# Kernel optimization log

Measured on AMD Instinct MI355X. Metric: run time of the kernel, lower is better.

## Reference

```python
import jax, jax.numpy as jnp
import numpy as np

N = 131072
K = 1024
D = 64

def setup_inputs() -> dict:
    key = jax.random.key(0)
    k1, k2 = jax.random.split(key)
    x = jax.random.normal(k1, (N, D), dtype=jnp.float32)
    emb_weight = jax.random.normal(k2, (K, D), dtype=jnp.float32)
    return {"x": x, "emb_weight": emb_weight}

def reference(x, emb_weight):
    distances = (
        jnp.sum(x * x, axis=1, keepdims=True)
        + jnp.sum(emb_weight * emb_weight, axis=1)
        - 2.0 * jnp.matmul(x, emb_weight.T)
    )
    codebook_indices = jnp.argmin(distances, axis=1)  # [N]
    probs = jax.nn.one_hot(codebook_indices, K, dtype=x.dtype)  # [N, K]
    z_q = emb_weight[codebook_indices]  # [N, D]
    return (z_q, probs)
```

## Files before the change

### kernel.cpp

```cpp
#include <hip/hip_runtime.h>
#include <math.h>

#define N_TOK 131072
#define K_CB  1024
#define D_DIM 64
#define MARGIN 0.03f

#define WS_EN     0
#define WS_ES     4096
#define WS_CNT    266240
#define WS_LIST   266256

typedef short bf16x8 __attribute__((ext_vector_type(8)));
typedef float f32x4  __attribute__((ext_vector_type(4)));

__device__ __forceinline__ ushort f2bf(float f) {
    uint u = __float_as_uint(f);
    u += 0x7FFFu + ((u >> 16) & 1u);
    return (ushort)(u >> 16);
}
__device__ __forceinline__ float bf2f(ushort h) {
    return __uint_as_float(((uint)h) << 16);
}

__global__ __launch_bounds__(256) void prep_fill(
    const float* __restrict__ emb, float* __restrict__ en,
    ushort* __restrict__ es, uint* __restrict__ fixcnt,
    float* __restrict__ probs)
{
    const int tid = threadIdx.x;
    const int b   = blockIdx.x;

    {
        const f32x4 z = {0.f, 0.f, 0.f, 0.f};
        f32x4* p = (f32x4*)probs + (size_t)b * 16384 + tid;
        #pragma unroll
        for (int i = 0; i < 64; ++i) p[(size_t)i * 256] = z;
    }

    if (b >= 16) return;

    const int c6   = tid & 63;
    const int q    = tid >> 6;
    const int code = b * 64 + c6;
    if (b == 0 && tid == 0) *fixcnt = 0;

    const int cb = code >> 4, jj = code & 15;
    const float* er = emb + (size_t)code * D_DIM;
    #pragma unroll
    for (int j = 0; j < 16; ++j) {
        int d = q * 16 + j;
        float f = er[d];
        ushort h = f2bf(f);
        ushort l = f2bf(f - bf2f(h));
        int ks = d >> 5, quad = (d >> 3) & 3, e = d & 7;
        es[(size_t)(((cb * 4 + ks)     * 4 + quad) * 16 + jj) * 8 + e] = h;
        es[(size_t)(((cb * 4 + ks + 2) * 4 + quad) * 16 + jj) * 8 + e] = l;
    }
    if (q == 0) {
        float s = 0.f;
        #pragma unroll
        for (int d = 0; d < D_DIM; ++d) s = fmaf(er[d], er[d], s);
        en[code] = s;
    }
}

__global__ __launch_bounds__(256) void vq_onehot(
    const float* __restrict__ x, const float* __restrict__ emb,
    const float* __restrict__ en, const ushort* __restrict__ es,
    float* __restrict__ zq, float* __restrict__ probs,
    uint* __restrict__ fixcnt, uint* __restrict__ fixlist, uint fixcap)
{
    const int tid  = threadIdx.x;
    const int wave = tid >> 6, lane = tid & 63;
    const int quad = lane >> 4, l15 = lane & 15;
    const int rg = wave >> 1;
    const int h  = wave & 1;
    const int blockRow = blockIdx.x * 64;
    const int waveRowBase = blockRow + rg * 32;

    __shared__ float lds_b1[2][64];
    __shared__ float lds_b2[2][64];
    __shared__ int   lds_k1[2][64];
    __shared__ int   lds_bk[64];

    bf16x8 af[2][4];
    #pragma unroll
    for (int g = 0; g < 2; ++g) {
        const float* xr = x + (size_t)(waveRowBase + g * 16 + l15) * D_DIM + quad * 8;
        f32x4 p0 = *(const f32x4*)(xr);
        f32x4 p1 = *(const f32x4*)(xr + 4);
        f32x4 p2 = *(const f32x4*)(xr + 32);
        f32x4 p3 = *(const f32x4*)(xr + 36);
        float v0[8], v1[8];
        #pragma unroll
        for (int j = 0; j < 4; ++j) { v0[j] = p0[j]; v0[4 + j] = p1[j]; v1[j] = p2[j]; v1[4 + j] = p3[j]; }
        #pragma unroll
        for (int j = 0; j < 8; ++j) {
            ushort h0 = f2bf(v0[j]);
            af[g][0][j] = (short)h0;
            af[g][2][j] = (short)f2bf(v0[j] - bf2f(h0));
            ushort h1 = f2bf(v1[j]);
            af[g][1][j] = (short)h1;
            af[g][3][j] = (short)f2bf(v1[j] - bf2f(h1));
        }
    }

    float b1[8], b2[8]; int k1[8];
    #pragma unroll
    for (int s = 0; s < 8; ++s) { b1[s] = INFINITY; b2[s] = INFINITY; k1[s] = 0; }

    const bf16x8* __restrict__ esv = (const bf16x8*)es;
    const int fidx = quad * 16 + l15;
    const int cb0  = h * 32;

    bf16x8 bc[4]; float enc;
    #pragma unroll
    for (int ks = 0; ks < 4; ++ks) bc[ks] = esv[(size_t)cb0 * 256 + ks * 64 + fidx];
    enc = en[cb0 * 16 + l15];

    #pragma unroll 2
    for (int i = 0; i < 32; ++i) {
        const int cb  = cb0 + i;
        const int nbi = cb0 + ((i + 1) & 31);
        bf16x8 bn[4]; float enn;
        #pragma unroll
        for (int ks = 0; ks < 4; ++ks) bn[ks] = esv[(size_t)nbi * 256 + ks * 64 + fidx];
        enn = en[nbi * 16 + l15];

        f32x4 acc0 = {0.f, 0.f, 0.f, 0.f};
        f32x4 acc1 = {0.f, 0.f, 0.f, 0.f};
        acc0 = __builtin_amdgcn_mfma_f32_16x16x32_bf16(af[0][0], bc[0], acc0, 0, 0, 0);
        acc0 = __builtin_amdgcn_mfma_f32_16x16x32_bf16(af[0][1], bc[1], acc0, 0, 0, 0);
        acc0 = __builtin_amdgcn_mfma_f32_16x16x32_bf16(af[0][0], bc[2], acc0, 0, 0, 0);
        acc0 = __builtin_amdgcn_mfma_f32_16x16x32_bf16(af[0][1], bc[3], acc0, 0, 0, 0);
        acc0 = __builtin_amdgcn_mfma_f32_16x16x32_bf16(af[0][2], bc[0], acc0, 0, 0, 0);
        acc0 = __builtin_amdgcn_mfma_f32_16x16x32_bf16(af[0][3], bc[1], acc0, 0, 0, 0);
        acc1 = __builtin_amdgcn_mfma_f32_16x16x32_bf16(af[1][0], bc[0], acc1, 0, 0, 0);
        acc1 = __builtin_amdgcn_mfma_f32_16x16x32_bf16(af[1][1], bc[1], acc1, 0, 0, 0);
        acc1 = __builtin_amdgcn_mfma_f32_16x16x32_bf16(af[1][0], bc[2], acc1, 0, 0, 0);
        acc1 = __builtin_amdgcn_mfma_f32_16x16x32_bf16(af[1][1], bc[3], acc1, 0, 0, 0);
        acc1 = __builtin_amdgcn_mfma_f32_16x16x32_bf16(af[1][2], bc[0], acc1, 0, 0, 0);
        acc1 = __builtin_amdgcn_mfma_f32_16x16x32_bf16(af[1][3], bc[1], acc1, 0, 0, 0);

        const int code = cb * 16 + l15;
        #pragma unroll
        for (int r = 0; r < 4; ++r) {
            {
                float d = fmaf(-2.f, acc0[r], enc);
                bool lt = d < b1[r];
                b2[r] = lt ? b1[r] : fminf(b2[r], d);
                k1[r] = lt ? code : k1[r];
                b1[r] = lt ? d : b1[r];
            }
            {
                int s = 4 + r;
                float d = fmaf(-2.f, acc1[r], enc);
                bool lt = d < b1[s];
                b2[s] = lt ? b1[s] : fminf(b2[s], d);
                k1[s] = lt ? code : k1[s];
                b1[s] = lt ? d : b1[s];
            }
        }

        #pragma unroll
        for (int ks = 0; ks < 4; ++ks) bc[ks] = bn[ks];
        enc = enn;
    }

    #pragma unroll
    for (int s = 0; s < 8; ++s) {
        #pragma unroll
        for (int off = 1; off < 16; off <<= 1) {
            float ob1 = __shfl_xor(b1[s], off);
            int   ok1 = __shfl_xor(k1[s], off);
            float ob2 = __shfl_xor(b2[s], off);
            bool better = (ob1 < b1[s]) || (ob1 == b1[s] && ok1 < k1[s]);
            float loser = better ? b1[s] : ob1;
            b1[s] = better ? ob1 : b1[s];
            k1[s] = better ? ok1 : k1[s];
            b2[s] = fminf(fminf(b2[s], ob2), loser);
        }
    }

    if (l15 == 0) {
        #pragma unroll
        for (int s = 0; s < 8; ++s) {
            int idx = rg * 32 + (s >> 2) * 16 + quad * 4 + (s & 3);
            lds_b1[h][idx] = b1[s];
            lds_b2[h][idx] = b2[s];
            lds_k1[h][idx] = k1[s];
        }
    }
    __syncthreads();

    if (tid < 64) {
        float a1 = lds_b1[0][tid], a2 = lds_b2[0][tid]; int ak = lds_k1[0][tid];
        float c1 = lds_b1[1][tid], c2 = lds_b2[1][tid]; int ck = lds_k1[1][tid];
        bool bwin = c1 < a1;
        float m1 = bwin ? c1 : a1;
        int   mk = bwin ? ck : ak;
        float loser = bwin ? a1 : c1;
        float m2 = fminf(fminf(a2, c2), loser);
        lds_bk[tid] = mk;
        probs[(size_t)(blockRow + tid) * K_CB + mk] = 1.0f;
        if (m2 - m1 <= MARGIN) {
            uint idx = atomicAdd(fixcnt, 1u);
            if (idx < fixcap) fixlist[idx] = (uint)(blockRow + tid) | ((uint)mk << 17);
        }
    }
    __syncthreads();

    #pragma unroll
    for (int mb = 0; mb < 4; ++mb) {
        int rl = wave * 16 + mb * 4 + quad;
        int bk = lds_bk[rl];
        f32x4 v = ((const f32x4*)(emb + (size_t)bk * D_DIM))[l15];
        ((f32x4*)(zq + (size_t)(blockRow + rl) * D_DIM))[l15] = v;
    }
}

__global__ __launch_bounds__(256) void vq_fixup(
    const float* __restrict__ x, const float* __restrict__ emb,
    const float* __restrict__ en,
    float* __restrict__ zq, float* __restrict__ probs,
    const uint* __restrict__ fixcnt, const uint* __restrict__ fixlist, uint fixcap)
{
    const int lane = threadIdx.x & 63;
    const int quad = lane >> 4, l15 = lane & 15;
    const uint gwave = (uint)((blockIdx.x * 256 + threadIdx.x) >> 6);
    uint cnt = *fixcnt;
    if (cnt > fixcap) cnt = fixcap;

    for (uint e = gwave; e < cnt; e += 1024u) {
        uint w = fixlist[e];
        int row = (int)(w & 0x1FFFFu);
        int kg  = (int)(w >> 17);

        const f32x4* xr4 = (const f32x4*)(x + (size_t)row * D_DIM) + quad * 4;
        f32x4 xv[4];
        #pragma unroll
        for (int c = 0; c < 4; ++c) xv[c] = xr4[c];
        float xn = 0.f;
        #pragma unroll
        for (int c = 0; c < 4; ++c)
            #pragma unroll
            for (int j = 0; j < 4; ++j) xn = fmaf(xv[c][j], xv[c][j], xn);
        xn += __shfl_xor(xn, 16);
        xn += __shfl_xor(xn, 32);

        float bd = INFINITY; int bk = 0;
        for (int t = 0; t < 64; ++t) {
            int code = t * 16 + l15;
            const f32x4* er4 = (const f32x4*)(emb + (size_t)code * D_DIM) + quad * 4;
            float dot = 0.f;
            #pragma unroll
            for (int c = 0; c < 4; ++c) {
                f32x4 ev = er4[c];
                #pragma unroll
                for (int j = 0; j < 4; ++j) dot = fmaf(xv[c][j], ev[j], dot);
            }
            dot += __shfl_xor(dot, 16);
            dot += __shfl_xor(dot, 32);
            float dist = fmaf(-2.f, dot, xn + en[code]);
            if (dist < bd) { bd = dist; bk = code; }
        }
        #pragma unroll
        for (int off = 1; off < 16; off <<= 1) {
            float od = __shfl_xor(bd, off);
            int   ok = __shfl_xor(bk, off);
            if (od < bd || (od == bd && ok < bk)) { bd = od; bk = ok; }
        }
        if (bk != kg) {
            if (lane == 0) {
                probs[(size_t)row * K_CB + kg] = 0.f;
                probs[(size_t)row * K_CB + bk] = 1.f;
            }
            if (lane < 16)
                ((f32x4*)(zq + (size_t)row * D_DIM))[lane] =
                    ((const f32x4*)(emb + (size_t)bk * D_DIM))[lane];
        }
    }
}

extern "C" void kernel_launch(void* const* d_in, const int* in_sizes, int n_in,
                              void* d_out, int out_size, void* d_ws, size_t ws_size,
                              hipStream_t stream) {
    const float* x   = (const float*)d_in[0];
    const float* emb = (const float*)d_in[1];
    float* zq    = (float*)d_out;
    float* probs = (float*)d_out + (size_t)N_TOK * D_DIM;

    char* ws = (char*)d_ws;
    float*  en      = (float*)(ws + WS_EN);
    ushort* es      = (ushort*)(ws + WS_ES);
    uint*   fixcnt  = (uint*)(ws + WS_CNT);
    uint*   fixlist = (uint*)(ws + WS_LIST);
    uint fixcap = (ws_size > WS_LIST + 4) ? (uint)((ws_size - WS_LIST) / 4) : 0u;

    prep_fill<<<2048, 256, 0, stream>>>(emb, en, es, fixcnt, probs);
    vq_onehot<<<N_TOK / 64, 256, 0, stream>>>(x, emb, en, es, zq, probs, fixcnt, fixlist, fixcap);
    vq_fixup<<<256, 256, 0, stream>>>(x, emb, en, zq, probs, fixcnt, fixlist, fixcap);
}
```

Measured before the change: 676.8 us.

## Fuse probs zero-fill into main VQ kernel and vectorize codebook prep

Moves the zeroing of the 512 MB one-hot probs buffer out of the prep kernel and into the main argmin kernel, where each block zeroes its own 64 rows before writing the one-hot entries. This lets the zero writes overlap with compute and shrinks prep to a small vectorized bf16 hi/lo split kernel. It also tightens the near-tie margin that sends rows to the fp32 fixup pass, so fewer rows get rechecked. A smaller margin raises the risk that bf16-split rounding picks the wrong code on close ties.

```diff
diff --git a/kernel.cpp b/kernel.cpp
--- a/kernel.cpp
+++ b/kernel.cpp
@@ -4,7 +4,7 @@
 #define N_TOK 131072
 #define K_CB  1024
 #define D_DIM 64
-#define MARGIN 0.03f
+#define MARGIN 0.008f
 
 #define WS_EN     0
 #define WS_ES     4096
@@ -23,45 +23,45 @@
     return __uint_as_float(((uint)h) << 16);
 }
 
-__global__ __launch_bounds__(256) void prep_fill(
+__global__ __launch_bounds__(256) void prep_kernel(
     const float* __restrict__ emb, float* __restrict__ en,
-    ushort* __restrict__ es, uint* __restrict__ fixcnt,
-    float* __restrict__ probs)
+    ushort* __restrict__ es, uint* __restrict__ fixcnt)
 {
     const int tid = threadIdx.x;
     const int b   = blockIdx.x;
-
-    {
-        const f32x4 z = {0.f, 0.f, 0.f, 0.f};
-        f32x4* p = (f32x4*)probs + (size_t)b * 16384 + tid;
-        #pragma unroll
-        for (int i = 0; i < 64; ++i) p[(size_t)i * 256] = z;
-    }
-
-    if (b >= 16) return;
-
-    const int c6   = tid & 63;
-    const int q    = tid >> 6;
-    const int code = b * 64 + c6;
     if (b == 0 && tid == 0) *fixcnt = 0;
 
-    const int cb = code >> 4, jj = code & 15;
-    const float* er = emb + (size_t)code * D_DIM;
-    #pragma unroll
-    for (int j = 0; j < 16; ++j) {
-        int d = q * 16 + j;
-        float f = er[d];
+    const int half = tid >> 7;
+    const int t    = tid & 127;
+    const int cb   = b * 2 + half;
+    const int jj   = t & 15;
+    const int quad = (t >> 4) & 3;
+    const int ks   = (t >> 6) & 1;
+    const int code = cb * 16 + jj;
+
+    const float* er = emb + (size_t)code * D_DIM + ks * 32 + quad * 8;
+    f32x4 pa = *(const f32x4*)(er);
+    f32x4 pb = *(const f32x4*)(er + 4);
+
+    bf16x8 hi, lo;
+    #pragma unroll
+    for (int j = 0; j < 8; ++j) {
+        float f = (j < 4) ? pa[j] : pb[j - 4];
         ushort h = f2bf(f);
-        ushort l = f2bf(f - bf2f(h));
-        int ks = d >> 5, quad = (d >> 3) & 3, e = d & 7;
-        es[(size_t)(((cb * 4 + ks)     * 4 + quad) * 16 + jj) * 8 + e] = h;
-        es[(size_t)(((cb * 4 + ks + 2) * 4 + quad) * 16 + jj) * 8 + e] = l;
-    }
-    if (q == 0) {
+        hi[j] = (short)h;
+        lo[j] = (short)f2bf(f - bf2f(h));
+    }
+    bf16x8* out = (bf16x8*)es;
+    out[(size_t)(cb * 4 + ks)     * 64 + quad * 16 + jj] = hi;
+    out[(size_t)(cb * 4 + ks + 2) * 64 + quad * 16 + jj] = lo;
+
+    if (tid < 32) {
+        const int c2 = b * 32 + tid;
+        const float* e2 = emb + (size_t)c2 * D_DIM;
         float s = 0.f;
         #pragma unroll
-        for (int d = 0; d < D_DIM; ++d) s = fmaf(er[d], er[d], s);
-        en[code] = s;
+        for (int d = 0; d < D_DIM; ++d) s = fmaf(e2[d], e2[d], s);
+        en[c2] = s;
     }
 }
 
@@ -203,7 +203,6 @@
         float loser = bwin ? a1 : c1;
         float m2 = fminf(fminf(a2, c2), loser);
         lds_bk[tid] = mk;
-        probs[(size_t)(blockRow + tid) * K_CB + mk] = 1.0f;
         if (m2 - m1 <= MARGIN) {
             uint idx = atomicAdd(fixcnt, 1u);
             if (idx < fixcap) fixlist[idx] = (uint)(blockRow + tid) | ((uint)mk << 17);
@@ -218,6 +217,19 @@
         f32x4 v = ((const f32x4*)(emb + (size_t)bk * D_DIM))[l15];
         ((f32x4*)(zq + (size_t)(blockRow + rl) * D_DIM))[l15] = v;
     }
+
+    const f32x4 zv = {0.f, 0.f, 0.f, 0.f};
+    for (int m = 0; m < 16; ++m) {
+        int rl = wave * 16 + m;
+        float* prow = probs + (size_t)(blockRow + rl) * K_CB;
+        #pragma unroll
+        for (int s = 0; s < 4; ++s)
+            *(f32x4*)(prow + s * 256 + lane * 4) = zv;
+    }
+    __syncthreads();
+
+    if (tid < 64)
+        probs[(size_t)(blockRow + tid) * K_CB + lds_bk[tid]] = 1.0f;
 }
 
 __global__ __launch_bounds__(256) void vq_fixup(
@@ -298,7 +310,7 @@
     uint*   fixlist = (uint*)(ws + WS_LIST);
     uint fixcap = (ws_size > WS_LIST + 4) ? (uint)((ws_size - WS_LIST) / 4) : 0u;
 
-    prep_fill<<<2048, 256, 0, stream>>>(emb, en, es, fixcnt, probs);
+    prep_kernel<<<32, 256, 0, stream>>>(emb, en, es, fixcnt);
     vq_onehot<<<N_TOK / 64, 256, 0, stream>>>(x, emb, en, es, zq, probs, fixcnt, fixlist, fixcap);
     vq_fixup<<<256, 256, 0, stream>>>(x, emb, en, zq, probs, fixcnt, fixlist, fixcap);
 }
```

Measured after the change: 648.1 us. 1.04x faster.
